# Kernel optimization log

Measured on AMD Instinct MI355X. Metric: run time of the kernel, lower is better.

Reference implementation:

```python
import jax, jax.numpy as jnp
import numpy as np

N_NODES = 50000


def setup_inputs() -> dict:
    key = jax.random.key(0)
    k1, k2, k3, k4, k5, k6 = jax.random.split(key, 6)
    c_in, c_out = 64, 64
    n_edges = 800000
    G = jax.random.normal(k1, (N_NODES, c_in), dtype=jnp.float32)
    RSC = jax.random.normal(k2, (N_NODES, c_in), dtype=jnp.float32)
    src = jax.random.randint(k3, (n_edges,), 0, N_NODES, dtype=jnp.int64)
    dst = jax.random.randint(k4, (n_edges,), 0, N_NODES, dtype=jnp.int64)
    W = jax.random.normal(k5, (c_out, c_in), dtype=jnp.float32) / np.sqrt(c_in)
    b = jax.random.normal(k6, (c_out,), dtype=jnp.float32) * 0.01
    return {"G": G, "RSC": RSC, "src": src, "dst": dst, "W": W, "b": b}


def reference(G, RSC, src, dst, W, b):
    # Per-edge relative feature: src node 'G' feature minus dst node 'RSC' feature
    rel = G[src] - RSC[dst]                          # [E, c_in]
    # Linear + ReLU (edge MLP)
    enc = jax.nn.relu(rel @ W.T + b)                 # [E, c_out]
    # Per-dst-node reductions over variable-size mailboxes
    max_agg = jax.ops.segment_max(enc, dst, num_segments=N_NODES)  # -inf for empty
    sum_agg = jax.ops.segment_sum(enc, dst, num_segments=N_NODES)
    cnt = jax.ops.segment_sum(jnp.ones_like(dst, dtype=enc.dtype), dst,
                              num_segments=N_NODES)               # [N]
    has_mail = (cnt > 0)[:, None]
    avg_agg = sum_agg / jnp.maximum(cnt, 1.0)[:, None]
    max_agg = jnp.where(has_mail, max_agg, 0.0)      # nodes w/o edges -> 0
    # concat(max, avg) as in reduce()
    return jnp.concatenate([max_agg, avg_agg], axis=-1)  # [N, 2*c_out]
```

## Files before the change

### kernel.cpp

```cpp
#include <hip/hip_runtime.h>
#include <hip/hip_bf16.h>

#define NCH 64
#define SPAN 64
#define BIN_BLOCKS 128
#define BIN_THREADS 1024
#define HIST_BLOCKS 256
#define SORT_CAP 3072

using bf16x8 = __attribute__((ext_vector_type(8))) short;
using f32x4 = __attribute__((ext_vector_type(4))) float;

__global__ void bucket_hist_kernel(const void* __restrict__ dstp,
                                   const unsigned short* __restrict__ gp, int n16,
                                   const unsigned* __restrict__ ip, int niw,
                                   unsigned* __restrict__ flags,
                                   unsigned* __restrict__ gcnt,
                                   int n_edges, int nb) {
    extern __shared__ unsigned lcnt[];
    unsigned* sodd = &lcnt[nb];
    for (int i = threadIdx.x; i < nb; i += blockDim.x) lcnt[i] = 0u;
    if (threadIdx.x == 0) *sodd = 0u;
    __syncthreads();
    unsigned lo = 0u;
    for (int i = threadIdx.x; i < niw; i += blockDim.x)
        if ((i & 1) && ip[i] != 0u) lo++;
    atomicAdd(sodd, lo);
    __syncthreads();
    const unsigned i64 = (*sodd < 50u) ? 1u : 0u;
    if (blockIdx.x == 0 && threadIdx.x == 0) flags[1] = i64;
    if (blockIdx.x == 0) {
        unsigned le = 0u;
        for (int i = threadIdx.x; i < n16; i += blockDim.x) {
            unsigned ex = (unsigned)((gp[i] >> 7) & 0xFFu);
            if (ex >= 0xC0u) le++;
        }
        __syncthreads();
        if (threadIdx.x == 0) *sodd = 0u;
        __syncthreads();
        atomicAdd(sodd, le);
        __syncthreads();
        if (threadIdx.x == 0) flags[0] = (*sodd > 50u) ? 1u : 0u;
    }
    const int stride = gridDim.x * blockDim.x;
    for (int e = blockIdx.x * blockDim.x + threadIdx.x; e < n_edges; e += stride) {
        int d = i64 ? (int)((const long long*)dstp)[e] : ((const int*)dstp)[e];
        atomicAdd(&lcnt[d >> 6], 1u);
    }
    __syncthreads();
    for (int i = threadIdx.x; i < nb; i += blockDim.x)
        if (lcnt[i]) atomicAdd(&gcnt[i], lcnt[i]);
}

__global__ void bucket_scan_kernel(const unsigned* __restrict__ gcnt,
                                   unsigned* __restrict__ boffs,
                                   unsigned* __restrict__ cursor, int nb) {
    __shared__ unsigned s[1024];
    const int t = threadIdx.x;
    const int L = (nb + 1023) / 1024;
    unsigned local = 0u;
    for (int i = 0; i < L; ++i) {
        int idx = t * L + i;
        if (idx < nb) local += gcnt[idx];
    }
    s[t] = local;
    __syncthreads();
    for (int off = 1; off < 1024; off <<= 1) {
        unsigned v = (t >= off) ? s[t - off] : 0u;
        __syncthreads();
        s[t] += v;
        __syncthreads();
    }
    unsigned run = s[t] - local;
    for (int i = 0; i < L; ++i) {
        int idx = t * L + i;
        if (idx < nb) { boffs[idx] = run; cursor[idx] = run; run += gcnt[idx]; }
    }
}

__global__ __launch_bounds__(BIN_THREADS)
void binning_kernel(const void* __restrict__ srcp, const void* __restrict__ dstp,
                    unsigned* __restrict__ cursor, unsigned* __restrict__ binned,
                    const unsigned* __restrict__ flags, int n_edges, int nb, int depth) {
    extern __shared__ unsigned lds[];
    unsigned* lcnt = lds;
    unsigned* stage = lds + nb;
    for (int i = threadIdx.x; i < nb; i += blockDim.x) lcnt[i] = 0u;
    __syncthreads();
    const unsigned i64 = flags[1];
    const int chunk = (n_edges + gridDim.x - 1) / gridDim.x;
    const int e0 = blockIdx.x * chunk;
    const int e1 = min(e0 + chunk, n_edges);
    for (int e = e0 + threadIdx.x; e < e1; e += blockDim.x) {
        int s, d;
        if (i64) {
            s = (int)((const long long*)srcp)[e];
            d = (int)((const long long*)dstp)[e];
        } else {
            s = ((const int*)srcp)[e];
            d = ((const int*)dstp)[e];
        }
        const int b = d >> 6;
        const unsigned pk = ((unsigned)(d & 63) << 26) | (unsigned)s;
        unsigned pos = atomicAdd(&lcnt[b], 1u);
        if ((int)pos < depth) {
            stage[b * depth + (int)pos] = pk;
        } else {
            unsigned g = atomicAdd(&cursor[b], 1u);
            binned[g] = pk;
        }
    }
    __syncthreads();
    for (int b = threadIdx.x; b < nb; b += blockDim.x) {
        int k = min((int)lcnt[b], depth);
        if (k > 0) {
            unsigned base = atomicAdd(&cursor[b], (unsigned)k);
            for (int i = 0; i < k; ++i) binned[base + i] = stage[b * depth + i];
        }
    }
}

__global__ __launch_bounds__(256)
void bucket_sort_kernel(const unsigned* __restrict__ binned,
                        const unsigned* __restrict__ boffs,
                        const unsigned* __restrict__ gcnt,
                        unsigned* __restrict__ sorted_src,
                        unsigned* __restrict__ offs,
                        int n_nodes, int n_edges, int nb) {
    __shared__ unsigned dcnt[SPAN];
    __shared__ unsigned doff[SPAN];
    __shared__ unsigned cur[SPAN];
    __shared__ unsigned stage[SORT_CAP];
    const int b = blockIdx.x;
    const int tid = threadIdx.x;
    const int estart = (int)boffs[b];
    const int count = (int)gcnt[b];

    if (tid < SPAN) dcnt[tid] = 0u;
    __syncthreads();

    for (int i = tid; i < count; i += 256) {
        const unsigned pk = binned[estart + i];
        atomicAdd(&dcnt[pk >> 26], 1u);
        if (i < SORT_CAP) stage[i] = pk;
    }
    __syncthreads();

    if (tid == 0) {
        unsigned run = 0u;
        #pragma unroll
        for (int i = 0; i < SPAN; ++i) { doff[i] = run; cur[i] = run; run += dcnt[i]; }
    }
    __syncthreads();

    if (tid < SPAN) {
        const int n = b * SPAN + tid;
        if (n < n_nodes) offs[n] = (unsigned)estart + doff[tid];
    }
    if (b == nb - 1 && tid == 0) offs[n_nodes] = (unsigned)n_edges;

    const int lim = (count < SORT_CAP) ? count : SORT_CAP;
    for (int i = tid; i < lim; i += 256) {
        const unsigned pk = stage[i];
        const unsigned pos = atomicAdd(&cur[pk >> 26], 1u);
        sorted_src[estart + pos] = pk & 0x03FFFFFFu;
    }
    for (int i = SORT_CAP + tid; i < count; i += 256) {
        const unsigned pk = binned[estart + i];
        const unsigned pos = atomicAdd(&cur[pk >> 26], 1u);
        sorted_src[estart + pos] = pk & 0x03FFFFFFu;
    }
}

__global__ __launch_bounds__(256)
void gemm2_kernel(const void* __restrict__ Gp, const void* __restrict__ Rp,
                  const void* __restrict__ Wp, const void* __restrict__ bp,
                  void* __restrict__ PQ,
                  const unsigned* __restrict__ flags, int n_nodes) {
    const unsigned f32 = flags[0];
    const int lane = threadIdx.x & 63;
    const int n_rows = 2 * n_nodes;

    if (!f32) {
        const unsigned short* Gh = (const unsigned short*)Gp;
        const unsigned short* Rh = (const unsigned short*)Rp;
        const unsigned short* Wh = (const unsigned short*)Wp;
        const __hip_bfloat16* bh = (const __hip_bfloat16*)bp;
        __hip_bfloat16* out = (__hip_bfloat16*)PQ;
        const int q = lane >> 4;
        const int mr = lane & 15;
        const int gwave = (blockIdx.x * blockDim.x + threadIdx.x) >> 6;
        const int nwaves = (gridDim.x * blockDim.x) >> 6;
        const int ngrp = (n_rows + 15) / 16;

        bf16x8 Bf[4][2];
        float bv[4];
        #pragma unroll
        for (int t = 0; t < 4; ++t) {
            const int c = t * 16 + mr;
            Bf[t][0] = *(const bf16x8*)(const void*)(Wh + (size_t)c * NCH + q * 8);
            Bf[t][1] = *(const bf16x8*)(const void*)(Wh + (size_t)c * NCH + 32 + q * 8);
            bv[t] = __bfloat162float(bh[c]);
        }

        auto rowptr = [&](int grp) -> const unsigned short* {
            int arow = grp * 16 + mr;
            if (arow >= n_rows) arow = n_rows - 1;
            return (arow < n_nodes) ? Gh + (size_t)arow * NCH
                                    : Rh + (size_t)(arow - n_nodes) * NCH;
        };

        bf16x8 A0, A1;
        if (gwave < ngrp) {
            const unsigned short* ap = rowptr(gwave);
            A0 = *(const bf16x8*)(const void*)(ap + q * 8);
            A1 = *(const bf16x8*)(const void*)(ap + 32 + q * 8);
        }
        for (int grp = gwave; grp < ngrp; grp += nwaves) {
            bf16x8 nA0, nA1;
            const int nxt = grp + nwaves;
            if (nxt < ngrp) {
                const unsigned short* ap = rowptr(nxt);
                nA0 = *(const bf16x8*)(const void*)(ap + q * 8);
                nA1 = *(const bf16x8*)(const void*)(ap + 32 + q * 8);
            }
            f32x4 acc0 = {0.f, 0.f, 0.f, 0.f}, acc1 = acc0, acc2 = acc0, acc3 = acc0;
            acc0 = __builtin_amdgcn_mfma_f32_16x16x32_bf16(A0, Bf[0][0], acc0, 0, 0, 0);
            acc1 = __builtin_amdgcn_mfma_f32_16x16x32_bf16(A0, Bf[1][0], acc1, 0, 0, 0);
            acc2 = __builtin_amdgcn_mfma_f32_16x16x32_bf16(A0, Bf[2][0], acc2, 0, 0, 0);
            acc3 = __builtin_amdgcn_mfma_f32_16x16x32_bf16(A0, Bf[3][0], acc3, 0, 0, 0);
            acc0 = __builtin_amdgcn_mfma_f32_16x16x32_bf16(A1, Bf[0][1], acc0, 0, 0, 0);
            acc1 = __builtin_amdgcn_mfma_f32_16x16x32_bf16(A1, Bf[1][1], acc1, 0, 0, 0);
            acc2 = __builtin_amdgcn_mfma_f32_16x16x32_bf16(A1, Bf[2][1], acc2, 0, 0, 0);
            acc3 = __builtin_amdgcn_mfma_f32_16x16x32_bf16(A1, Bf[3][1], acc3, 0, 0, 0);
            const int m0 = grp * 16;
            #pragma unroll
            for (int r = 0; r < 4; ++r) {
                const int row = m0 + q * 4 + r;
                if (row < n_rows) {
                    const bool isQ = (row >= n_nodes);
                    const size_t rb = (size_t)row * NCH + mr;
                    out[rb +  0] = __float2bfloat16(acc0[r] - (isQ ? bv[0] : 0.f));
                    out[rb + 16] = __float2bfloat16(acc1[r] - (isQ ? bv[1] : 0.f));
                    out[rb + 32] = __float2bfloat16(acc2[r] - (isQ ? bv[2] : 0.f));
                    out[rb + 48] = __float2bfloat16(acc3[r] - (isQ ? bv[3] : 0.f));
                }
            }
            A0 = nA0; A1 = nA1;
        }
        return;
    }

    const int waveInBlk = threadIdx.x >> 6;
    const int wavesPerBlk = blockDim.x >> 6;
    const int gwave = blockIdx.x * wavesPerBlk + waveInBlk;
    const int nwaves = gridDim.x * wavesPerBlk;
    const int ngroups = (n_rows + 3) / 4;

    __shared__ float ldsb[4 * 4 * NCH];
    float* slot = &ldsb[waveInBlk * 4 * NCH];

    float w[NCH];
    const float* Wf = (const float*)Wp;
    #pragma unroll
    for (int k = 0; k < NCH; ++k) w[k] = Wf[lane * NCH + k];
    const float bias = ((const float*)bp)[lane];

    const int niter = (ngroups + nwaves - 1) / nwaves;
    for (int it = 0; it < niter; ++it) {
        const int grp = gwave + it * nwaves;
        const bool gvalid = (grp < ngroups);
        const int m0 = grp * 4;
        if (gvalid) {
            const int myrow = m0 + (lane >> 4);
            const int col = (lane & 15) * 4;
            float x0 = 0.f, x1 = 0.f, x2 = 0.f, x3 = 0.f;
            if (myrow < n_rows) {
                const bool isQ = (myrow >= n_nodes);
                const int r = isQ ? (myrow - n_nodes) : myrow;
                const float* inp = (const float*)(isQ ? Rp : Gp);
                float4 v = *(const float4*)(inp + (size_t)r * NCH + col);
                x0 = v.x; x1 = v.y; x2 = v.z; x3 = v.w;
            }
            const int sb = (lane >> 4) * NCH + col;
            slot[sb + 0] = x0; slot[sb + 1] = x1; slot[sb + 2] = x2; slot[sb + 3] = x3;
        }
        __syncthreads();
        if (gvalid) {
            #pragma unroll
            for (int rr = 0; rr < 4; ++rr) {
                const int m = m0 + rr;
                if (m < n_rows) {
                    float a0 = 0.f, a1 = 0.f, a2 = 0.f, a3 = 0.f;
                    const float4* r4 = (const float4*)(slot + rr * NCH);
                    #pragma unroll
                    for (int qq = 0; qq < 16; ++qq) {
                        float4 rv = r4[qq];
                        a0 = fmaf(rv.x, w[4 * qq + 0], a0);
                        a1 = fmaf(rv.y, w[4 * qq + 1], a1);
                        a2 = fmaf(rv.z, w[4 * qq + 2], a2);
                        a3 = fmaf(rv.w, w[4 * qq + 3], a3);
                    }
                    float acc = (a0 + a1) + (a2 + a3);
                    if (m >= n_nodes) acc -= bias;
                    ((float*)PQ)[(size_t)m * NCH + lane] = acc;
                }
            }
        }
        __syncthreads();
    }
}

__global__ void node_kernel(const void* __restrict__ PQ,
                            const unsigned* __restrict__ sorted_src,
                            const unsigned* __restrict__ offs,
                            const unsigned* __restrict__ flags,
                            void* __restrict__ outp, int n_nodes) {
    const unsigned f32 = flags[0];
    const int lane = threadIdx.x & 63;
    const int gwave = (blockIdx.x * blockDim.x + threadIdx.x) >> 6;
    const int nwaves = (gridDim.x * blockDim.x) >> 6;
    const float* Pf = (const float*)PQ;
    const unsigned short* Ph = (const unsigned short*)PQ;

    for (int n = gwave; n < n_nodes; n += nwaves) {
        float q;
        if (f32) q = Pf[(size_t)(n_nodes + n) * NCH + lane];
        else {
            unsigned short h = Ph[(size_t)(n_nodes + n) * NCH + lane];
            q = __bfloat162float(*(__hip_bfloat16*)&h);
        }
        const int start = (int)offs[n];
        const int end = (int)offs[n + 1];
        float vmax = 0.0f, vsum = 0.0f;
        int j = start;
        for (; j + 8 <= end; j += 8) {
            int s[8];
            #pragma unroll
            for (int u = 0; u < 8; ++u) s[u] = (int)sorted_src[j + u];
            float p[8];
            if (f32) {
                #pragma unroll
                for (int u = 0; u < 8; ++u) p[u] = Pf[(size_t)s[u] * NCH + lane];
            } else {
                unsigned short h[8];
                #pragma unroll
                for (int u = 0; u < 8; ++u) h[u] = Ph[(size_t)s[u] * NCH + lane];
                #pragma unroll
                for (int u = 0; u < 8; ++u) p[u] = __bfloat162float(*(__hip_bfloat16*)&h[u]);
            }
            #pragma unroll
            for (int u = 0; u < 8; ++u) {
                const float v = fmaxf(p[u] - q, 0.0f);
                vmax = fmaxf(vmax, v);
                vsum += v;
            }
        }
        for (; j < end; ++j) {
            const int s = (int)sorted_src[j];
            float p;
            if (f32) p = Pf[(size_t)s * NCH + lane];
            else {
                unsigned short h = Ph[(size_t)s * NCH + lane];
                p = __bfloat162float(*(__hip_bfloat16*)&h);
            }
            const float v = fmaxf(p - q, 0.0f);
            vmax = fmaxf(vmax, v);
            vsum += v;
        }
        const int deg = end - start;
        const float avg = vsum / (float)(deg > 0 ? deg : 1);
        if (f32) {
            float* out = (float*)outp;
            out[(size_t)n * 2 * NCH + lane] = vmax;
            out[(size_t)n * 2 * NCH + NCH + lane] = avg;
        } else {
            __hip_bfloat16* out = (__hip_bfloat16*)outp;
            out[(size_t)n * 2 * NCH + lane] = __float2bfloat16(vmax);
            out[(size_t)n * 2 * NCH + NCH + lane] = __float2bfloat16(avg);
        }
    }
}

extern "C" void kernel_launch(void* const* d_in, const int* in_sizes, int n_in,
                              void* d_out, int out_size, void* d_ws, size_t ws_size,
                              hipStream_t stream) {
    const void* G = d_in[0];
    const void* RSC = d_in[1];
    const void* src = d_in[2];
    const void* dst = d_in[3];
    const void* W = d_in[4];
    const void* b = d_in[5];

    const int n_nodes = in_sizes[0] / NCH;
    const int n_edges = in_sizes[2];
    const int nb = (n_nodes + SPAN - 1) / SPAN;

    char* ws = (char*)d_ws;
    unsigned* flags = (unsigned*)ws;
    size_t off = 256;
    unsigned* binned = (unsigned*)(ws + off);
    off += (((size_t)n_edges * 4 + 255) / 256) * 256;
    unsigned* sorted_src = (unsigned*)(ws + off);
    off += (((size_t)n_edges * 4 + 255) / 256) * 256;
    unsigned* offs = (unsigned*)(ws + off);
    off += (((size_t)(n_nodes + 1) * 4 + 255) / 256) * 256;
    unsigned* boffs = (unsigned*)(ws + off);
    off += (((size_t)nb * 4 + 255) / 256) * 256;
    unsigned* cursor = (unsigned*)(ws + off);
    off += (((size_t)nb * 4 + 255) / 256) * 256;
    unsigned* gcnt = (unsigned*)(ws + off);
    off += (((size_t)nb * 4 + 255) / 256) * 256;
    void* PQ = (void*)(ws + off);

    const int n_g_probe = (in_sizes[0] < 8192) ? in_sizes[0] : 8192;
    const int n_idx_probe = (n_edges < 8192) ? n_edges : 8192;

    hipMemsetAsync(gcnt, 0, (size_t)nb * 4, stream);

    bucket_hist_kernel<<<HIST_BLOCKS, 256, (size_t)(nb + 1) * 4, stream>>>(
        dst, (const unsigned short*)G, n_g_probe, (const unsigned*)src, n_idx_probe,
        flags, gcnt, n_edges, nb);

    bucket_scan_kernel<<<1, 1024, 0, stream>>>(gcnt, boffs, cursor, nb);

    int depth = 16384 / nb - 1;
    if (depth > 19) depth = 19;
    if (depth < 4) depth = 4;
    const size_t bin_lds = (size_t)nb * (depth + 1) * 4;
    binning_kernel<<<BIN_BLOCKS, BIN_THREADS, bin_lds, stream>>>(
        src, dst, cursor, binned, flags, n_edges, nb, depth);

    bucket_sort_kernel<<<nb, 256, 0, stream>>>(binned, boffs, gcnt, sorted_src,
                                               offs, n_nodes, n_edges, nb);

    gemm2_kernel<<<512, 256, 0, stream>>>(G, RSC, W, b, PQ, flags, n_nodes);

    node_kernel<<<2048, 256, 0, stream>>>(PQ, sorted_src, offs, flags, d_out, n_nodes);
}
```

Baseline: 200.3 us.

## Fuse histogram with scan, binning with GEMM, and bucket sort with node aggregation

The separate scan kernel is merged into the histogram kernel: the last block to finish, detected with an atomic counter, performs the prefix scan. Binning and the P/Q projection GEMM now run in one launch, with some blocks doing binning and the rest doing the GEMM. The per-bucket counting sort now happens in LDS inside the node aggregation kernel, which removes the sorted_src and offs global arrays and their round trip. The fp32 GEMM path is simplified to a per-wave row loop that reads W from memory instead of registers, which may cost throughput, and buckets with more edges than the LDS capacity fall back to a slow rescan.

```diff
diff --git a/kernel.cpp b/kernel.cpp
--- a/kernel.cpp
+++ b/kernel.cpp
@@ -3,183 +3,142 @@
 
 #define NCH 64
 #define SPAN 64
-#define BIN_BLOCKS 128
-#define BIN_THREADS 1024
+#define FUSE_BIN 128
+#define FUSE_GEMM 128
 #define HIST_BLOCKS 256
-#define SORT_CAP 3072
+#define SORT_CAP 2048
 
 using bf16x8 = __attribute__((ext_vector_type(8))) short;
 using f32x4 = __attribute__((ext_vector_type(4))) float;
 
-__global__ void bucket_hist_kernel(const void* __restrict__ dstp,
-                                   const unsigned short* __restrict__ gp, int n16,
-                                   const unsigned* __restrict__ ip, int niw,
-                                   unsigned* __restrict__ flags,
-                                   unsigned* __restrict__ gcnt,
-                                   int n_edges, int nb) {
+__global__ void hist_scan_kernel(const void* __restrict__ dstp,
+                                 const unsigned short* __restrict__ gp, int n16,
+                                 const unsigned* __restrict__ ip, int niw,
+                                 unsigned* __restrict__ flags,
+                                 unsigned* __restrict__ gcnt,
+                                 unsigned* __restrict__ boffs,
+                                 unsigned* __restrict__ cursor,
+                                 int n_edges, int nb) {
     extern __shared__ unsigned lcnt[];
+    __shared__ unsigned ss[256];
+    __shared__ unsigned isLast;
     unsigned* sodd = &lcnt[nb];
-    for (int i = threadIdx.x; i < nb; i += blockDim.x) lcnt[i] = 0u;
-    if (threadIdx.x == 0) *sodd = 0u;
+    const int tid = threadIdx.x;
+    for (int i = tid; i < nb; i += blockDim.x) lcnt[i] = 0u;
+    if (tid == 0) *sodd = 0u;
     __syncthreads();
     unsigned lo = 0u;
-    for (int i = threadIdx.x; i < niw; i += blockDim.x)
+    for (int i = tid; i < niw; i += blockDim.x)
         if ((i & 1) && ip[i] != 0u) lo++;
     atomicAdd(sodd, lo);
     __syncthreads();
     const unsigned i64 = (*sodd < 50u) ? 1u : 0u;
-    if (blockIdx.x == 0 && threadIdx.x == 0) flags[1] = i64;
+    if (blockIdx.x == 0 && tid == 0) flags[1] = i64;
     if (blockIdx.x == 0) {
         unsigned le = 0u;
-        for (int i = threadIdx.x; i < n16; i += blockDim.x) {
+        for (int i = tid; i < n16; i += blockDim.x) {
             unsigned ex = (unsigned)((gp[i] >> 7) & 0xFFu);
             if (ex >= 0xC0u) le++;
         }
         __syncthreads();
-        if (threadIdx.x == 0) *sodd = 0u;
+        if (tid == 0) *sodd = 0u;
         __syncthreads();
         atomicAdd(sodd, le);
         __syncthreads();
-        if (threadIdx.x == 0) flags[0] = (*sodd > 50u) ? 1u : 0u;
+        if (tid == 0) flags[0] = (*sodd > 50u) ? 1u : 0u;
     }
     const int stride = gridDim.x * blockDim.x;
-    for (int e = blockIdx.x * blockDim.x + threadIdx.x; e < n_edges; e += stride) {
+    for (int e = blockIdx.x * blockDim.x + tid; e < n_edges; e += stride) {
         int d = i64 ? (int)((const long long*)dstp)[e] : ((const int*)dstp)[e];
         atomicAdd(&lcnt[d >> 6], 1u);
     }
     __syncthreads();
-    for (int i = threadIdx.x; i < nb; i += blockDim.x)
+    for (int i = tid; i < nb; i += blockDim.x)
         if (lcnt[i]) atomicAdd(&gcnt[i], lcnt[i]);
-}
-
-__global__ void bucket_scan_kernel(const unsigned* __restrict__ gcnt,
-                                   unsigned* __restrict__ boffs,
-                                   unsigned* __restrict__ cursor, int nb) {
-    __shared__ unsigned s[1024];
-    const int t = threadIdx.x;
-    const int L = (nb + 1023) / 1024;
+    __threadfence();
+    __syncthreads();
+    if (tid == 0)
+        isLast = (atomicAdd(&gcnt[nb], 1u) == (unsigned)(gridDim.x - 1)) ? 1u : 0u;
+    __syncthreads();
+    if (!isLast) return;
+    __threadfence();
+    const int L = (nb + 255) / 256;
+    const int base = tid * L;
     unsigned local = 0u;
     for (int i = 0; i < L; ++i) {
-        int idx = t * L + i;
+        int idx = base + i;
         if (idx < nb) local += gcnt[idx];
     }
-    s[t] = local;
-    __syncthreads();
-    for (int off = 1; off < 1024; off <<= 1) {
-        unsigned v = (t >= off) ? s[t - off] : 0u;
-        __syncthreads();
-        s[t] += v;
-        __syncthreads();
-    }
-    unsigned run = s[t] - local;
+    ss[tid] = local;
+    __syncthreads();
+    #pragma unroll
+    for (int o = 1; o < 256; o <<= 1) {
+        unsigned v = (tid >= o) ? ss[tid - o] : 0u;
+        __syncthreads();
+        ss[tid] += v;
+        __syncthreads();
+    }
+    unsigned run = ss[tid] - local;
     for (int i = 0; i < L; ++i) {
-        int idx = t * L + i;
+        int idx = base + i;
         if (idx < nb) { boffs[idx] = run; cursor[idx] = run; run += gcnt[idx]; }
     }
 }
 
-__global__ __launch_bounds__(BIN_THREADS)
-void binning_kernel(const void* __restrict__ srcp, const void* __restrict__ dstp,
-                    unsigned* __restrict__ cursor, unsigned* __restrict__ binned,
-                    const unsigned* __restrict__ flags, int n_edges, int nb, int depth) {
-    extern __shared__ unsigned lds[];
-    unsigned* lcnt = lds;
-    unsigned* stage = lds + nb;
-    for (int i = threadIdx.x; i < nb; i += blockDim.x) lcnt[i] = 0u;
-    __syncthreads();
-    const unsigned i64 = flags[1];
-    const int chunk = (n_edges + gridDim.x - 1) / gridDim.x;
-    const int e0 = blockIdx.x * chunk;
-    const int e1 = min(e0 + chunk, n_edges);
-    for (int e = e0 + threadIdx.x; e < e1; e += blockDim.x) {
-        int s, d;
-        if (i64) {
-            s = (int)((const long long*)srcp)[e];
-            d = (int)((const long long*)dstp)[e];
-        } else {
-            s = ((const int*)srcp)[e];
-            d = ((const int*)dstp)[e];
-        }
-        const int b = d >> 6;
-        const unsigned pk = ((unsigned)(d & 63) << 26) | (unsigned)s;
-        unsigned pos = atomicAdd(&lcnt[b], 1u);
-        if ((int)pos < depth) {
-            stage[b * depth + (int)pos] = pk;
-        } else {
-            unsigned g = atomicAdd(&cursor[b], 1u);
-            binned[g] = pk;
-        }
-    }
-    __syncthreads();
-    for (int b = threadIdx.x; b < nb; b += blockDim.x) {
-        int k = min((int)lcnt[b], depth);
-        if (k > 0) {
-            unsigned base = atomicAdd(&cursor[b], (unsigned)k);
-            for (int i = 0; i < k; ++i) binned[base + i] = stage[b * depth + i];
-        }
-    }
-}
-
-__global__ __launch_bounds__(256)
-void bucket_sort_kernel(const unsigned* __restrict__ binned,
-                        const unsigned* __restrict__ boffs,
-                        const unsigned* __restrict__ gcnt,
-                        unsigned* __restrict__ sorted_src,
-                        unsigned* __restrict__ offs,
-                        int n_nodes, int n_edges, int nb) {
-    __shared__ unsigned dcnt[SPAN];
-    __shared__ unsigned doff[SPAN];
-    __shared__ unsigned cur[SPAN];
-    __shared__ unsigned stage[SORT_CAP];
-    const int b = blockIdx.x;
-    const int tid = threadIdx.x;
-    const int estart = (int)boffs[b];
-    const int count = (int)gcnt[b];
-
-    if (tid < SPAN) dcnt[tid] = 0u;
-    __syncthreads();
-
-    for (int i = tid; i < count; i += 256) {
-        const unsigned pk = binned[estart + i];
-        atomicAdd(&dcnt[pk >> 26], 1u);
-        if (i < SORT_CAP) stage[i] = pk;
-    }
-    __syncthreads();
-
-    if (tid == 0) {
-        unsigned run = 0u;
-        #pragma unroll
-        for (int i = 0; i < SPAN; ++i) { doff[i] = run; cur[i] = run; run += dcnt[i]; }
-    }
-    __syncthreads();
-
-    if (tid < SPAN) {
-        const int n = b * SPAN + tid;
-        if (n < n_nodes) offs[n] = (unsigned)estart + doff[tid];
-    }
-    if (b == nb - 1 && tid == 0) offs[n_nodes] = (unsigned)n_edges;
-
-    const int lim = (count < SORT_CAP) ? count : SORT_CAP;
-    for (int i = tid; i < lim; i += 256) {
-        const unsigned pk = stage[i];
-        const unsigned pos = atomicAdd(&cur[pk >> 26], 1u);
-        sorted_src[estart + pos] = pk & 0x03FFFFFFu;
-    }
-    for (int i = SORT_CAP + tid; i < count; i += 256) {
-        const unsigned pk = binned[estart + i];
-        const unsigned pos = atomicAdd(&cur[pk >> 26], 1u);
-        sorted_src[estart + pos] = pk & 0x03FFFFFFu;
-    }
-}
-
-__global__ __launch_bounds__(256)
-void gemm2_kernel(const void* __restrict__ Gp, const void* __restrict__ Rp,
-                  const void* __restrict__ Wp, const void* __restrict__ bp,
-                  void* __restrict__ PQ,
-                  const unsigned* __restrict__ flags, int n_nodes) {
+__global__ __launch_bounds__(1024)
+void bin_gemm_kernel(const void* __restrict__ srcp, const void* __restrict__ dstp,
+                     unsigned* __restrict__ cursor, unsigned* __restrict__ binned,
+                     const void* __restrict__ Gp, const void* __restrict__ Rp,
+                     const void* __restrict__ Wp, const void* __restrict__ bp,
+                     void* __restrict__ PQ,
+                     const unsigned* __restrict__ flags,
+                     int n_edges, int nb, int depth, int n_nodes) {
     const unsigned f32 = flags[0];
+    const int n_rows = 2 * n_nodes;
+
+    if (blockIdx.x < FUSE_BIN) {
+        extern __shared__ unsigned lds[];
+        unsigned* lcnt = lds;
+        unsigned* stage = lds + nb;
+        for (int i = threadIdx.x; i < nb; i += blockDim.x) lcnt[i] = 0u;
+        __syncthreads();
+        const unsigned i64 = flags[1];
+        const int chunk = (n_edges + FUSE_BIN - 1) / FUSE_BIN;
+        const int e0 = blockIdx.x * chunk;
+        const int e1 = min(e0 + chunk, n_edges);
+        for (int e = e0 + threadIdx.x; e < e1; e += blockDim.x) {
+            int s, d;
+            if (i64) {
+                s = (int)((const long long*)srcp)[e];
+                d = (int)((const long long*)dstp)[e];
+            } else {
+                s = ((const int*)srcp)[e];
+                d = ((const int*)dstp)[e];
+            }
+            const int b = d >> 6;
+            const unsigned pk = ((unsigned)(d & 63) << 26) | (unsigned)s;
+            unsigned pos = atomicAdd(&lcnt[b], 1u);
+            if ((int)pos < depth) {
+                stage[b * depth + (int)pos] = pk;
+            } else {
+                unsigned g = atomicAdd(&cursor[b], 1u);
+                binned[g] = pk;
+            }
+        }
+        __syncthreads();
+        for (int b = threadIdx.x; b < nb; b += blockDim.x) {
+            int k = min((int)lcnt[b], depth);
+            if (k > 0) {
+                unsigned base = atomicAdd(&cursor[b], (unsigned)k);
+                for (int i = 0; i < k; ++i) binned[base + i] = stage[b * depth + i];
+            }
+        }
+        return;
+    }
+
     const int lane = threadIdx.x & 63;
-    const int n_rows = 2 * n_nodes;
+    const int gwave = (blockIdx.x - FUSE_BIN) * 16 + (threadIdx.x >> 6);
+    const int nwaves = FUSE_GEMM * 16;
 
     if (!f32) {
         const unsigned short* Gh = (const unsigned short*)Gp;
@@ -189,8 +148,6 @@
         __hip_bfloat16* out = (__hip_bfloat16*)PQ;
         const int q = lane >> 4;
         const int mr = lane & 15;
-        const int gwave = (blockIdx.x * blockDim.x + threadIdx.x) >> 6;
-        const int nwaves = (gridDim.x * blockDim.x) >> 6;
         const int ngrp = (n_rows + 15) / 16;
 
         bf16x8 Bf[4][2];
@@ -251,93 +208,77 @@
         return;
     }
 
-    const int waveInBlk = threadIdx.x >> 6;
-    const int wavesPerBlk = blockDim.x >> 6;
-    const int gwave = blockIdx.x * wavesPerBlk + waveInBlk;
-    const int nwaves = gridDim.x * wavesPerBlk;
-    const int ngroups = (n_rows + 3) / 4;
-
-    __shared__ float ldsb[4 * 4 * NCH];
-    float* slot = &ldsb[waveInBlk * 4 * NCH];
-
-    float w[NCH];
     const float* Wf = (const float*)Wp;
-    #pragma unroll
-    for (int k = 0; k < NCH; ++k) w[k] = Wf[lane * NCH + k];
     const float bias = ((const float*)bp)[lane];
-
-    const int niter = (ngroups + nwaves - 1) / nwaves;
-    for (int it = 0; it < niter; ++it) {
-        const int grp = gwave + it * nwaves;
-        const bool gvalid = (grp < ngroups);
-        const int m0 = grp * 4;
-        if (gvalid) {
-            const int myrow = m0 + (lane >> 4);
-            const int col = (lane & 15) * 4;
-            float x0 = 0.f, x1 = 0.f, x2 = 0.f, x3 = 0.f;
-            if (myrow < n_rows) {
-                const bool isQ = (myrow >= n_nodes);
-                const int r = isQ ? (myrow - n_nodes) : myrow;
-                const float* inp = (const float*)(isQ ? Rp : Gp);
-                float4 v = *(const float4*)(inp + (size_t)r * NCH + col);
-                x0 = v.x; x1 = v.y; x2 = v.z; x3 = v.w;
-            }
-            const int sb = (lane >> 4) * NCH + col;
-            slot[sb + 0] = x0; slot[sb + 1] = x1; slot[sb + 2] = x2; slot[sb + 3] = x3;
-        }
-        __syncthreads();
-        if (gvalid) {
-            #pragma unroll
-            for (int rr = 0; rr < 4; ++rr) {
-                const int m = m0 + rr;
-                if (m < n_rows) {
-                    float a0 = 0.f, a1 = 0.f, a2 = 0.f, a3 = 0.f;
-                    const float4* r4 = (const float4*)(slot + rr * NCH);
-                    #pragma unroll
-                    for (int qq = 0; qq < 16; ++qq) {
-                        float4 rv = r4[qq];
-                        a0 = fmaf(rv.x, w[4 * qq + 0], a0);
-                        a1 = fmaf(rv.y, w[4 * qq + 1], a1);
-                        a2 = fmaf(rv.z, w[4 * qq + 2], a2);
-                        a3 = fmaf(rv.w, w[4 * qq + 3], a3);
-                    }
-                    float acc = (a0 + a1) + (a2 + a3);
-                    if (m >= n_nodes) acc -= bias;
-                    ((float*)PQ)[(size_t)m * NCH + lane] = acc;
-                }
-            }
-        }
-        __syncthreads();
+    for (int m = gwave; m < n_rows; m += nwaves) {
+        const float* inp = (m < n_nodes)
+            ? (const float*)Gp + (size_t)m * NCH
+            : (const float*)Rp + (size_t)(m - n_nodes) * NCH;
+        float acc = 0.0f;
+        #pragma unroll
+        for (int k = 0; k < NCH; ++k) acc = fmaf(inp[k], Wf[lane * NCH + k], acc);
+        if (m >= n_nodes) acc -= bias;
+        ((float*)PQ)[(size_t)m * NCH + lane] = acc;
     }
 }
 
-__global__ void node_kernel(const void* __restrict__ PQ,
-                            const unsigned* __restrict__ sorted_src,
-                            const unsigned* __restrict__ offs,
-                            const unsigned* __restrict__ flags,
-                            void* __restrict__ outp, int n_nodes) {
+__global__ __launch_bounds__(256)
+void bucket_node_kernel(const void* __restrict__ PQ,
+                        const unsigned* __restrict__ binned,
+                        const unsigned* __restrict__ boffs,
+                        const unsigned* __restrict__ gcnt,
+                        const unsigned* __restrict__ flags,
+                        void* __restrict__ outp, int n_nodes) {
+    __shared__ unsigned dcnt[SPAN];
+    __shared__ unsigned doff[SPAN];
+    __shared__ unsigned cur[SPAN];
+    __shared__ unsigned sl[SORT_CAP];
     const unsigned f32 = flags[0];
-    const int lane = threadIdx.x & 63;
-    const int gwave = (blockIdx.x * blockDim.x + threadIdx.x) >> 6;
-    const int nwaves = (gridDim.x * blockDim.x) >> 6;
+    const int b = blockIdx.x;
+    const int tid = threadIdx.x;
+    const int estart = (int)boffs[b];
+    const int count = (int)gcnt[b];
+    const int lim = (count < SORT_CAP) ? count : SORT_CAP;
     const float* Pf = (const float*)PQ;
     const unsigned short* Ph = (const unsigned short*)PQ;
 
-    for (int n = gwave; n < n_nodes; n += nwaves) {
+    if (tid < SPAN) dcnt[tid] = 0u;
+    __syncthreads();
+    for (int i = tid; i < lim; i += 256)
+        atomicAdd(&dcnt[binned[estart + i] >> 26], 1u);
+    __syncthreads();
+    if (tid == 0) {
+        unsigned run = 0u;
+        #pragma unroll
+        for (int i = 0; i < SPAN; ++i) { doff[i] = run; cur[i] = run; run += dcnt[i]; }
+    }
+    __syncthreads();
+    for (int i = tid; i < lim; i += 256) {
+        const unsigned pk = binned[estart + i];
+        const unsigned pos = atomicAdd(&cur[pk >> 26], 1u);
+        sl[pos] = pk & 0x03FFFFFFu;
+    }
+    __syncthreads();
+
+    const int lane = tid & 63;
+    const int w = tid >> 6;
+    for (int li = w * 16; li < w * 16 + 16; ++li) {
+        const int n = b * SPAN + li;
+        if (n >= n_nodes) continue;
         float q;
         if (f32) q = Pf[(size_t)(n_nodes + n) * NCH + lane];
         else {
             unsigned short h = Ph[(size_t)(n_nodes + n) * NCH + lane];
             q = __bfloat162float(*(__hip_bfloat16*)&h);
         }
-        const int start = (int)offs[n];
-        const int end = (int)offs[n + 1];
+        const int start = (int)doff[li];
+        const int end = start + (int)dcnt[li];
         float vmax = 0.0f, vsum = 0.0f;
         int j = start;
         for (; j + 8 <= end; j += 8) {
             int s[8];
             #pragma unroll
-            for (int u = 0; u < 8; ++u) s[u] = (int)sorted_src[j + u];
+            for (int u = 0; u < 8; ++u) s[u] = (int)sl[j + u];
             float p[8];
             if (f32) {
                 #pragma unroll
@@ -347,7 +288,8 @@
                 #pragma unroll
                 for (int u = 0; u < 8; ++u) h[u] = Ph[(size_t)s[u] * NCH + lane];
                 #pragma unroll
-                for (int u = 0; u < 8; ++u) p[u] = __bfloat162float(*(__hip_bfloat16*)&h[u]);
+                for (int u = 0; u < 8; ++u)
+                    p[u] = __bfloat162float(*(__hip_bfloat16*)&h[u]);
             }
             #pragma unroll
             for (int u = 0; u < 8; ++u) {
@@ -357,7 +299,7 @@
             }
         }
         for (; j < end; ++j) {
-            const int s = (int)sorted_src[j];
+            const int s = (int)sl[j];
             float p;
             if (f32) p = Pf[(size_t)s * NCH + lane];
             else {
@@ -368,7 +310,25 @@
             vmax = fmaxf(vmax, v);
             vsum += v;
         }
-        const int deg = end - start;
+        int deg = end - start;
+        if (count > SORT_CAP) {
+            for (int j2 = SORT_CAP; j2 < count; ++j2) {
+                const unsigned pk = binned[estart + j2];
+                if ((int)(pk >> 26) == li) {
+                    const int s = (int)(pk & 0x03FFFFFFu);
+                    float p;
+                    if (f32) p = Pf[(size_t)s * NCH + lane];
+                    else {
+                        unsigned short h = Ph[(size_t)s * NCH + lane];
+                        p = __bfloat162float(*(__hip_bfloat16*)&h);
+                    }
+                    const float v = fmaxf(p - q, 0.0f);
+                    vmax = fmaxf(vmax, v);
+                    vsum += v;
+                    deg++;
+                }
+            }
+        }
         const float avg = vsum / (float)(deg > 0 ? deg : 1);
         if (f32) {
             float* out = (float*)outp;
@@ -401,40 +361,31 @@
     size_t off = 256;
     unsigned* binned = (unsigned*)(ws + off);
     off += (((size_t)n_edges * 4 + 255) / 256) * 256;
-    unsigned* sorted_src = (unsigned*)(ws + off);
-    off += (((size_t)n_edges * 4 + 255) / 256) * 256;
-    unsigned* offs = (unsigned*)(ws + off);
-    off += (((size_t)(n_nodes + 1) * 4 + 255) / 256) * 256;
     unsigned* boffs = (unsigned*)(ws + off);
     off += (((size_t)nb * 4 + 255) / 256) * 256;
     unsigned* cursor = (unsigned*)(ws + off);
     off += (((size_t)nb * 4 + 255) / 256) * 256;
     unsigned* gcnt = (unsigned*)(ws + off);
-    off += (((size_t)nb * 4 + 255) / 256) * 256;
+    off += (((size_t)(nb + 1) * 4 + 255) / 256) * 256;
     void* PQ = (void*)(ws + off);
 
     const int n_g_probe = (in_sizes[0] < 8192) ? in_sizes[0] : 8192;
     const int n_idx_probe = (n_edges < 8192) ? n_edges : 8192;
 
-    hipMemsetAsync(gcnt, 0, (size_t)nb * 4, stream);
-
-    bucket_hist_kernel<<<HIST_BLOCKS, 256, (size_t)(nb + 1) * 4, stream>>>(
+    hipMemsetAsync(gcnt, 0, (size_t)(nb + 1) * 4, stream);
+
+    hist_scan_kernel<<<HIST_BLOCKS, 256, (size_t)(nb + 1) * 4, stream>>>(
         dst, (const unsigned short*)G, n_g_probe, (const unsigned*)src, n_idx_probe,
-        flags, gcnt, n_edges, nb);
-
-    bucket_scan_kernel<<<1, 1024, 0, stream>>>(gcnt, boffs, cursor, nb);
+        flags, gcnt, boffs, cursor, n_edges, nb);
 
     int depth = 16384 / nb - 1;
     if (depth > 19) depth = 19;
     if (depth < 4) depth = 4;
     const size_t bin_lds = (size_t)nb * (depth + 1) * 4;
-    binning_kernel<<<BIN_BLOCKS, BIN_THREADS, bin_lds, stream>>>(
-        src, dst, cursor, binned, flags, n_edges, nb, depth);
-
-    bucket_sort_kernel<<<nb, 256, 0, stream>>>(binned, boffs, gcnt, sorted_src,
-                                               offs, n_nodes, n_edges, nb);
-
-    gemm2_kernel<<<512, 256, 0, stream>>>(G, RSC, W, b, PQ, flags, n_nodes);
-
-    node_kernel<<<2048, 256, 0, stream>>>(PQ, sorted_src, offs, flags, d_out, n_nodes);
+    bin_gemm_kernel<<<FUSE_BIN + FUSE_GEMM, 1024, bin_lds, stream>>>(
+        src, dst, cursor, binned, G, RSC, W, b, PQ, flags,
+        n_edges, nb, depth, n_nodes);
+
+    bucket_node_kernel<<<nb, 256, 0, stream>>>(PQ, binned, boffs, gcnt, flags,
+                                               d_out, n_nodes);
 }
```

After: 630.3 us. +214.6%, slower.
